# Performance work log

Hardware: AMD Instinct MI355X
Metric: run time of the kernel (lower is better)

Reference implementation:

```python
import jax, jax.numpy as jnp
import numpy as np

N = 100000
NEG_SLOPE = 0.2
EPS = 1e-16


def _gat_layer(x, W, a_src, a_dst, b, src, dst, heads, dim, concat):
    # Linear projection -> [N, H, D]
    h = (x @ W).reshape(x.shape[0], heads, dim)
    # Per-node attention logits [N, H]
    al_src = jnp.sum(h * a_src[None], axis=-1)
    al_dst = jnp.sum(h * a_dst[None], axis=-1)
    # Per-edge logits, leaky relu (negative_slope=0.2)
    e = al_src[src] + al_dst[dst]                      # [E, H]
    e = jnp.where(e >= 0, e, NEG_SLOPE * e)
    # Scatter softmax over destination neighborhoods
    emax = jax.ops.segment_max(e, dst, num_segments=N)  # [N, H]
    ee = jnp.exp(e - emax[dst])
    denom = jax.ops.segment_sum(ee, dst, num_segments=N)
    alpha = ee / (denom[dst] + EPS)                    # [E, H]
    # Weighted scatter-add aggregation
    msg = h[src] * alpha[:, :, None]                   # [E, H, D]
    out = jax.ops.segment_sum(msg, dst, num_segments=N)  # [N, H, D]
    if concat:
        out = out.reshape(N, heads * dim)
    else:
        out = out.mean(axis=1)
    return out + b


def setup_inputs() -> dict:
    key = jax.random.key(0)
    ks = jax.random.split(key, 10)
    F_in, hid, H, C = 500, 8, 8, 3
    E = 3200000
    x = jax.random.normal(ks[0], (N, F_in), dtype=jnp.float32)
    edge_index = jax.random.randint(ks[1], (2, E), 0, N, dtype=jnp.int64)
    s1 = (1.0 / np.sqrt(F_in)).astype(np.float32)
    s2 = (1.0 / np.sqrt(hid * H)).astype(np.float32)
    return {
        "x": x,
        "edge_index": edge_index,
        "W1": jax.random.normal(ks[2], (F_in, H * hid), dtype=jnp.float32) * s1,
        "att_src1": jax.random.normal(ks[3], (H, hid), dtype=jnp.float32),
        "att_dst1": jax.random.normal(ks[4], (H, hid), dtype=jnp.float32),
        "b1": jnp.zeros((H * hid,), dtype=jnp.float32),
        "W2": jax.random.normal(ks[5], (H * hid, C), dtype=jnp.float32) * s2,
        "att_src2": jax.random.normal(ks[6], (1, C), dtype=jnp.float32),
        "att_dst2": jax.random.normal(ks[7], (1, C), dtype=jnp.float32),
        "b2": jnp.zeros((C,), dtype=jnp.float32),
    }


def reference(x, edge_index, W1, att_src1, att_dst1, b1, W2, att_src2, att_dst2, b2):
    # Add self-loops (PyG GATConv default)
    loop = jnp.arange(N, dtype=edge_index.dtype)
    src = jnp.concatenate([edge_index[0], loop])
    dst = jnp.concatenate([edge_index[1], loop])
    # Layer 1: 8 heads, concat -> [N, 64], ELU
    h = _gat_layer(x, W1, att_src1, att_dst1, b1, src, dst, heads=8, dim=8, concat=True)
    h = jax.nn.elu(h)
    # Layer 2: 1 head, no concat -> [N, 3]
    out = _gat_layer(h, W2, att_src2, att_dst2, b2, src, dst, heads=1, dim=3, concat=False)
    return out, jax.nn.log_softmax(out, axis=1)
```

## Files before the change

### kernel.cpp

```cpp
#include <hip/hip_runtime.h>
#include <hip/hip_bf16.h>


#define F_IN 500
#define HEADS 8
#define HID 8
#define HD 64
#define CLS 3
#define NEG 0.2f
#define EPSV 1e-16f
#define LOG2E 1.44269504088896340736f

#define NBLK_H 128
#define NBKT_MAX 3136

typedef __attribute__((ext_vector_type(8))) short short8v;
typedef __attribute__((ext_vector_type(4))) float f32x4;

__device__ inline short bfs(float v) {
    __hip_bfloat16 b = __float2bfloat16(v);
    return *(short*)&b;
}

__device__ inline int ld_edge(const void* ei, long idx, int is64) {
    return is64 ? (int)((const long long*)ei)[idx] : ((const int*)ei)[idx];
}

__global__ void k_prepW(const float* __restrict__ W1, ushort* __restrict__ W1b2,
                        const int* __restrict__ ei, int* __restrict__ flag) {
    if (blockIdx.x == 0 && threadIdx.x == 0) {
        int z = 0;
        for (int i = 1; i < 16; i += 2) z += (ei[i] == 0) ? 1 : 0;
        *flag = (z == 8) ? 1 : 0;
    }
    int i = blockIdx.x * 256 + threadIdx.x;
    if (i >= 16 * 64 * 32) return;
    int ks = i >> 11;
    int c = (i >> 5) & 63;
    int st = i & 31;
    int q = (st >> 3) ^ ((c >> 1) & 3);
    int k = ks * 32 + q * 8 + (st & 7);
    float v = (k < F_IN) ? W1[k * HD + c] : 0.f;
    __hip_bfloat16 b = __float2bfloat16(v);
    W1b2[i] = *(ushort*)&b;
}

__device__ __forceinline__ void g1_stage(const float* __restrict__ x,
        const ushort* __restrict__ W1b2, char* smem, int buf, int ks,
        int rowb, int N, int lane, int w) {
    const int k0 = ks * 32;
    {
        const ushort* srcB = W1b2 + ks * 2048 + (w * 64 + lane) * 8;
        char* dstB = smem + 16384 + buf * 4096 + w * 1024;
        __builtin_amdgcn_global_load_lds(
            (const __attribute__((address_space(1))) void*)srcB,
            (__attribute__((address_space(3))) void*)dstB, 16, 0, 0);
    }
#pragma unroll
    for (int i = 0; i < 2; ++i) {
        int vt = i * 256 + w * 64 + lane;
        int row = vt >> 3;
        int c = (vt & 7) ^ (row & 7);
        int ke = k0 + c * 4; if (ke > 496) ke = 496;
        int rowg = rowb + row; if (rowg >= N) rowg = N - 1;
        const float* srcA = x + (long)rowg * F_IN + ke;
        char* dstA = smem + buf * 8192 + i * 4096 + w * 1024;
        __builtin_amdgcn_global_load_lds(
            (const __attribute__((address_space(1))) void*)srcA,
            (__attribute__((address_space(3))) void*)dstA, 16, 0, 0);
    }
}

__global__ __launch_bounds__(256) void k_gemm1(const float* __restrict__ x,
        const ushort* __restrict__ W1b2,
        const float* __restrict__ asrc, const float* __restrict__ adst,
        float* __restrict__ als, float* __restrict__ ald,
        ushort* __restrict__ h1b, int N) {
    __shared__ char smem[24576];
    int t = threadIdx.x;
    int lane = t & 63;
    int w = t >> 6;
    int l16 = lane & 15, oct = lane >> 4;
    int rowb = blockIdx.x * 64;

    f32x4 acc0 = {0.f, 0.f, 0.f, 0.f};
    f32x4 acc1 = {0.f, 0.f, 0.f, 0.f};
    f32x4 acc2 = {0.f, 0.f, 0.f, 0.f};
    f32x4 acc3 = {0.f, 0.f, 0.f, 0.f};

    g1_stage(x, W1b2, smem, 0, 0, rowb, N, lane, w);
    __syncthreads();

    int rl = w * 16 + l16;
    int asw = l16 & 7;
    int bsw = (l16 >> 1) & 3;

    for (int ks = 0; ks < 16; ++ks) {
        int cur = ks & 1;
        if (ks < 15)
            g1_stage(x, W1b2, smem, cur ^ 1, ks + 1, rowb, N, lane, w);
        const char* Ab = smem + cur * 8192;
        const char* Bb = smem + 16384 + cur * 4096;
        float4 x0 = *reinterpret_cast<const float4*>(
            Ab + rl * 128 + ((2 * oct + 0) ^ asw) * 16);
        float4 x1 = *reinterpret_cast<const float4*>(
            Ab + rl * 128 + ((2 * oct + 1) ^ asw) * 16);
        short8v a;
        a[0] = bfs(x0.x); a[1] = bfs(x0.y); a[2] = bfs(x0.z); a[3] = bfs(x0.w);
        a[4] = bfs(x1.x); a[5] = bfs(x1.y); a[6] = bfs(x1.z); a[7] = bfs(x1.w);
        short8v b0 = *reinterpret_cast<const short8v*>(
            Bb + (0 * 16 + l16) * 64 + (oct ^ bsw) * 16);
        short8v b1 = *reinterpret_cast<const short8v*>(
            Bb + (1 * 16 + l16) * 64 + (oct ^ bsw) * 16);
        short8v b2 = *reinterpret_cast<const short8v*>(
            Bb + (2 * 16 + l16) * 64 + (oct ^ bsw) * 16);
        short8v b3 = *reinterpret_cast<const short8v*>(
            Bb + (3 * 16 + l16) * 64 + (oct ^ bsw) * 16);
        acc0 = __builtin_amdgcn_mfma_f32_16x16x32_bf16(a, b0, acc0, 0, 0, 0);
        acc1 = __builtin_amdgcn_mfma_f32_16x16x32_bf16(a, b1, acc1, 0, 0, 0);
        acc2 = __builtin_amdgcn_mfma_f32_16x16x32_bf16(a, b2, acc2, 0, 0, 0);
        acc3 = __builtin_amdgcn_mfma_f32_16x16x32_bf16(a, b3, acc3, 0, 0, 0);
        __syncthreads();
    }

    float* fs = (float*)smem;
#pragma unroll
    for (int r = 0; r < 4; ++r) {
        int rl_ = w * 16 + oct * 4 + r;
        fs[rl_ * 64 + l16 +  0] = acc0[r];
        fs[rl_ * 64 + l16 + 16] = acc1[r];
        fs[rl_ * 64 + l16 + 32] = acc2[r];
        fs[rl_ * 64 + l16 + 48] = acc3[r];
    }
    __syncthreads();
#pragma unroll
    for (int j = t; j < 512; j += 256) {
        int row = j >> 3, h = j & 7;
        int gn = rowb + row;
        if (gn < N) {
            const float* hp = fs + row * 64 + h * 8;
            float4 v0 = *reinterpret_cast<const float4*>(hp);
            float4 v1 = *reinterpret_cast<const float4*>(hp + 4);
            const float* s = asrc + h * 8;
            const float* d = adst + h * 8;
            float s1 = v0.x * s[0] + v0.y * s[1] + v0.z * s[2] + v0.w * s[3]
                     + v1.x * s[4] + v1.y * s[5] + v1.z * s[6] + v1.w * s[7];
            float s2 = v0.x * d[0] + v0.y * d[1] + v0.z * d[2] + v0.w * d[3]
                     + v1.x * d[4] + v1.y * d[5] + v1.z * d[6] + v1.w * d[7];
            als[gn * 8 + h] = s1 * LOG2E;
            ald[gn * 8 + h] = s2 * LOG2E;
            ushort hb[8];
            hb[0] = (ushort)bfs(v0.x); hb[1] = (ushort)bfs(v0.y);
            hb[2] = (ushort)bfs(v0.z); hb[3] = (ushort)bfs(v0.w);
            hb[4] = (ushort)bfs(v1.x); hb[5] = (ushort)bfs(v1.y);
            hb[6] = (ushort)bfs(v1.z); hb[7] = (ushort)bfs(v1.w);
            *reinterpret_cast<uint4*>(h1b + (long)gn * HD + h * 8) =
                *reinterpret_cast<const uint4*>(hb);
        }
    }
}


__global__ __launch_bounds__(256) void k_hist(const void* ei, int E, int N, int nbkt,
        int* __restrict__ ghist, const int* flag) {
    __shared__ int h[NBKT_MAX];
    int tot = E + N;
    int epb = (tot + NBLK_H - 1) / NBLK_H;
    int e0 = blockIdx.x * epb, e1 = min(tot, e0 + epb);
    for (int i = threadIdx.x; i < nbkt; i += 256) h[i] = 0;
    __syncthreads();
    int is64 = *flag;
    for (int e = e0 + threadIdx.x; e < e1; e += 256) {
        int dst = (e < E) ? ld_edge(ei, (long)E + e, is64) : (e - E);
        atomicAdd(&h[dst >> 5], 1);
    }
    __syncthreads();
    for (int i = threadIdx.x; i < nbkt; i += 256)
        ghist[blockIdx.x * nbkt + i] = h[i];
}

__global__ void k_bsum(const int* __restrict__ ghist, int* __restrict__ colsum, int nbkt) {
    int b = blockIdx.x * 256 + threadIdx.x;
    if (b >= nbkt) return;
    int s = 0;
    for (int i = 0; i < NBLK_H; i++) s += ghist[i * nbkt + b];
    colsum[b] = s;
}

__global__ __launch_bounds__(256) void k_bscan2(const int* __restrict__ colsum,
        int* __restrict__ boff, int nbkt) {
    __shared__ int part[256];
    int per = (nbkt + 255) / 256;
    int t = threadIdx.x;
    int lo = t * per, hi = min(nbkt, lo + per);
    int s = 0;
    for (int i = lo; i < hi; i++) s += colsum[i];
    part[t] = s;
    __syncthreads();
    for (int off = 1; off < 256; off <<= 1) {
        int v = (t >= off) ? part[t - off] : 0;
        __syncthreads();
        part[t] += v;
        __syncthreads();
    }
    int run = (t > 0) ? part[t - 1] : 0;
    for (int i = lo; i < hi; i++) { boff[i] = run; run += colsum[i]; }
    if (t == 255) boff[nbkt] = part[255];
}

__global__ void k_bapply(int* __restrict__ ghist, const int* __restrict__ boff, int nbkt) {
    int b = blockIdx.x * 256 + threadIdx.x;
    if (b >= nbkt) return;
    int run = boff[b];
    for (int i = 0; i < NBLK_H; i++) {
        int v = ghist[i * nbkt + b];
        ghist[i * nbkt + b] = run;
        run += v;
    }
}

__global__ __launch_bounds__(256) void k_scatter(const void* ei, int E, int N, int nbkt,
        const int* __restrict__ ghist, uint* __restrict__ pairs, const int* flag) {
    __shared__ int cur[NBKT_MAX];
    int tot = E + N;
    int epb = (tot + NBLK_H - 1) / NBLK_H;
    int e0 = blockIdx.x * epb, e1 = min(tot, e0 + epb);
    for (int i = threadIdx.x; i < nbkt; i += 256) cur[i] = ghist[blockIdx.x * nbkt + i];
    __syncthreads();
    int is64 = *flag;
    for (int e = e0 + threadIdx.x; e < e1; e += 256) {
        int src, dst;
        if (e < E) { src = ld_edge(ei, e, is64); dst = ld_edge(ei, (long)E + e, is64); }
        else { src = dst = e - E; }
        int pos = atomicAdd(&cur[dst >> 5], 1);
        pairs[pos] = ((uint)src << 5) | (uint)(dst & 31);
    }
}

__global__ __launch_bounds__(256) void k_fill3(const uint* __restrict__ pairs,
        const int* __restrict__ boff, int* __restrict__ rowptr,
        int* __restrict__ csr, int N, int nbkt) {
    __shared__ int cnt[32];
    __shared__ int base[32];
    __shared__ int cur[32];
    int b = blockIdx.x;
    int t = threadIdx.x;
    if (t < 32) { cnt[t] = 0; cur[t] = 0; }
    __syncthreads();
    int p0 = boff[b], p1 = boff[b + 1];
    for (int p = p0 + t; p < p1; p += 256)
        atomicAdd(&cnt[pairs[p] & 31], 1);
    __syncthreads();
    if (t < 32) {
        int pre = 0;
#pragma unroll
        for (int i = 0; i < 32; i++) pre += (i < t) ? cnt[i] : 0;
        base[t] = p0 + pre;
        int n = b * 32 + t;
        if (n < N) rowptr[n] = base[t];
    }
    if (b == 0 && t == 0) rowptr[N] = boff[nbkt];
    __syncthreads();
    for (int p = p0 + t; p < p1; p += 256) {
        uint v = pairs[p];
        int lo = v & 31;
        int pos = base[lo] + atomicAdd(&cur[lo], 1);
        csr[pos] = (int)(v >> 5);
    }
}

__global__ __launch_bounds__(256) void k_agg1(const int* __restrict__ rowptr,
        const int* __restrict__ csr, const ushort* __restrict__ h1b,
        const float* __restrict__ als, const float* __restrict__ ald,
        const float* __restrict__ b1, const float* __restrict__ W2,
        const float* __restrict__ as2, const float* __restrict__ ad2,
        float* __restrict__ h2p, float* __restrict__ als2,
        float* __restrict__ ald2, int N) {
    int n = blockIdx.x * 4 + (threadIdx.x >> 6);
    if (n >= N) return;
    int lane = threadIdx.x & 63;
    int es = lane >> 3;
    int h = lane & 7;
    float aldh = ald[n * HEADS + h];
    int rs = rowptr[n], re = rowptr[n + 1];

    float a0 = 0.f, a1 = 0.f, a2 = 0.f, a3 = 0.f;
    float a4 = 0.f, a5 = 0.f, a6 = 0.f, a7 = 0.f;
    float c0 = 0.f, c1 = 0.f, c2 = 0.f, c3 = 0.f;
    float c4 = 0.f, c5 = 0.f, c6 = 0.f, c7 = 0.f;
    float den = 0.f, den2 = 0.f;

    int jb = rs;
    for (; jb + 16 <= re; jb += 16) {
        int sA = csr[jb + es];
        int sB = csr[jb + 8 + es];
        float eA = als[sA * HEADS + h] + aldh;
        float eB = als[sB * HEADS + h] + aldh;
        uint4 uA = *reinterpret_cast<const uint4*>(h1b + (long)sA * HD + h * 8);
        uint4 uB = *reinterpret_cast<const uint4*>(h1b + (long)sB * HD + h * 8);
        eA = fmaxf(eA, NEG * eA);
        eB = fmaxf(eB, NEG * eB);
        float pA = exp2f(eA);
        float pB = exp2f(eB);
        a0 += pA * __uint_as_float(uA.x << 16);
        a1 += pA * __uint_as_float(uA.x & 0xffff0000u);
        a2 += pA * __uint_as_float(uA.y << 16);
        a3 += pA * __uint_as_float(uA.y & 0xffff0000u);
        a4 += pA * __uint_as_float(uA.z << 16);
        a5 += pA * __uint_as_float(uA.z & 0xffff0000u);
        a6 += pA * __uint_as_float(uA.w << 16);
        a7 += pA * __uint_as_float(uA.w & 0xffff0000u);
        den += pA;
        c0 += pB * __uint_as_float(uB.x << 16);
        c1 += pB * __uint_as_float(uB.x & 0xffff0000u);
        c2 += pB * __uint_as_float(uB.y << 16);
        c3 += pB * __uint_as_float(uB.y & 0xffff0000u);
        c4 += pB * __uint_as_float(uB.z << 16);
        c5 += pB * __uint_as_float(uB.z & 0xffff0000u);
        c6 += pB * __uint_as_float(uB.w << 16);
        c7 += pB * __uint_as_float(uB.w & 0xffff0000u);
        den2 += pB;
    }
    for (; jb < re; jb += 8) {
        int eidx = jb + es;
        bool valid = (eidx < re);
        int s = csr[valid ? eidx : rs];
        float e = als[s * HEADS + h] + aldh;
        e = fmaxf(e, NEG * e);
        float p = valid ? exp2f(e) : 0.f;
        uint4 u = *reinterpret_cast<const uint4*>(h1b + (long)s * HD + h * 8);
        a0 += p * __uint_as_float(u.x << 16);
        a1 += p * __uint_as_float(u.x & 0xffff0000u);
        a2 += p * __uint_as_float(u.y << 16);
        a3 += p * __uint_as_float(u.y & 0xffff0000u);
        a4 += p * __uint_as_float(u.z << 16);
        a5 += p * __uint_as_float(u.z & 0xffff0000u);
        a6 += p * __uint_as_float(u.w << 16);
        a7 += p * __uint_as_float(u.w & 0xffff0000u);
        den += p;
    }
    a0 += c0; a1 += c1; a2 += c2; a3 += c3;
    a4 += c4; a5 += c5; a6 += c6; a7 += c7;
    den += den2;
#pragma unroll
    for (int off = 8; off < 64; off <<= 1) {
        den += __shfl_xor(den, off);
        a0 += __shfl_xor(a0, off); a1 += __shfl_xor(a1, off);
        a2 += __shfl_xor(a2, off); a3 += __shfl_xor(a3, off);
        a4 += __shfl_xor(a4, off); a5 += __shfl_xor(a5, off);
        a6 += __shfl_xor(a6, off); a7 += __shfl_xor(a7, off);
    }
    float sel = (es < 4)
        ? ((es < 2) ? ((es == 0) ? a0 : a1) : ((es == 2) ? a2 : a3))
        : ((es < 6) ? ((es == 4) ? a4 : a5) : ((es == 6) ? a6 : a7));
    int d = h * 8 + es;
    float o = sel / (den + EPSV) + b1[d];
    o = (o > 0.f) ? o : __expf(o) - 1.f;
    float p0 = o * W2[d * CLS + 0];
    float p1 = o * W2[d * CLS + 1];
    float p2 = o * W2[d * CLS + 2];
#pragma unroll
    for (int off = 1; off < 64; off <<= 1) {
        p0 += __shfl_xor(p0, off);
        p1 += __shfl_xor(p1, off);
        p2 += __shfl_xor(p2, off);
    }
    if (lane == 0) {
        *reinterpret_cast<float4*>(h2p + (long)n * 4) = make_float4(p0, p1, p2, 0.f);
        als2[n] = (p0 * as2[0] + p1 * as2[1] + p2 * as2[2]) * LOG2E;
        ald2[n] = (p0 * ad2[0] + p1 * ad2[1] + p2 * ad2[2]) * LOG2E;
    }
}

__global__ __launch_bounds__(256) void k_agg2(const int* __restrict__ rowptr,
        const int* __restrict__ csr, const float* __restrict__ h2p,
        const float* __restrict__ als2v, const float* __restrict__ ald2v,
        const float* __restrict__ b2, float* __restrict__ out, int N) {
    int n = blockIdx.x * 8 + (threadIdx.x >> 5);
    if (n >= N) return;
    int lane = threadIdx.x & 31;
    float aldv = ald2v[n];
    int rs = rowptr[n], re = rowptr[n + 1];
    float sum = 0.f, a0 = 0.f, a1 = 0.f, a2 = 0.f;
    for (int j = rs + lane; j < re; j += 32) {
        int s = csr[j];
        float e = als2v[s] + aldv;
        e = fmaxf(e, NEG * e);
        float p = exp2f(e);
        float4 hv = *reinterpret_cast<const float4*>(h2p + (long)s * 4);
        sum += p;
        a0 += p * hv.x;
        a1 += p * hv.y;
        a2 += p * hv.z;
    }
#pragma unroll
    for (int off = 1; off < 32; off <<= 1) {
        sum += __shfl_xor(sum, off);
        a0 += __shfl_xor(a0, off);
        a1 += __shfl_xor(a1, off);
        a2 += __shfl_xor(a2, off);
    }
    if (lane == 0) {
        float d = sum + EPSV;
        float v0 = a0 / d + b2[0], v1 = a1 / d + b2[1], v2 = a2 / d + b2[2];
        float mx = fmaxf(v0, fmaxf(v1, v2));
        float se = __expf(v0 - mx) + __expf(v1 - mx) + __expf(v2 - mx);
        float ls = mx + __logf(se);
        out[n * CLS + 0] = v0; out[n * CLS + 1] = v1; out[n * CLS + 2] = v2;
        long o2 = (long)N * CLS;
        out[o2 + n * CLS + 0] = v0 - ls;
        out[o2 + n * CLS + 1] = v1 - ls;
        out[o2 + n * CLS + 2] = v2 - ls;
    }
}

extern "C" void kernel_launch(void* const* d_in, const int* in_sizes, int n_in,
                              void* d_out, int out_size, void* d_ws, size_t ws_size,
                              hipStream_t stream) {
    const float* x   = (const float*)d_in[0];
    const void*  ei  = d_in[1];
    const float* W1  = (const float*)d_in[2];
    const float* as1 = (const float*)d_in[3];
    const float* ad1 = (const float*)d_in[4];
    const float* b1  = (const float*)d_in[5];
    const float* W2  = (const float*)d_in[6];
    const float* as2 = (const float*)d_in[7];
    const float* ad2 = (const float*)d_in[8];
    const float* b2  = (const float*)d_in[9];
    int N = in_sizes[0] / F_IN;
    int E = in_sizes[1] / 2;
    int tot = E + N;
    int nbkt = (N + 31) >> 5;

    char* w = (char*)d_ws;
    auto alloc = [&](size_t bytes) -> char* {
        char* p = w; w += (bytes + 255) & ~size_t(255); return p;
    };
    ushort* h1b    = (ushort*)alloc((size_t)N * HD * 2);
    float*  als1   = (float*)alloc((size_t)N * HEADS * 4);
    float*  ald1   = (float*)alloc((size_t)N * HEADS * 4);
    int*    rowptr = (int*)alloc((size_t)(N + 1) * 4);
    int*    csr    = (int*)alloc((size_t)tot * 4);
    float*  h2p    = (float*)alloc((size_t)N * 4 * 4);
    float*  als2   = (float*)alloc((size_t)N * 4);
    float*  ald2   = (float*)alloc((size_t)N * 4);
    ushort* W1b2   = (ushort*)alloc((size_t)16 * 64 * 32 * 2);
    int*    flag   = (int*)alloc(256);
    uint*   pairs  = (uint*)alloc((size_t)tot * 4);
    int*    ghist  = (int*)alloc((size_t)NBLK_H * nbkt * 4);
    int*    colsum = (int*)alloc((size_t)nbkt * 4);
    int*    boff   = (int*)alloc((size_t)(nbkt + 1) * 4);

    k_prepW<<<(16 * 64 * 32 + 255) / 256, 256, 0, stream>>>(W1, W1b2, (const int*)ei, flag);
    k_gemm1<<<(N + 63) / 64, 256, 0, stream>>>(x, W1b2, as1, ad1, als1, ald1, h1b, N);
    k_hist<<<NBLK_H, 256, 0, stream>>>(ei, E, N, nbkt, ghist, flag);
    k_bsum<<<(nbkt + 255) / 256, 256, 0, stream>>>(ghist, colsum, nbkt);
    k_bscan2<<<1, 256, 0, stream>>>(colsum, boff, nbkt);
    k_bapply<<<(nbkt + 255) / 256, 256, 0, stream>>>(ghist, boff, nbkt);
    k_scatter<<<NBLK_H, 256, 0, stream>>>(ei, E, N, nbkt, ghist, pairs, flag);
    k_fill3<<<nbkt, 256, 0, stream>>>(pairs, boff, rowptr, csr, N, nbkt);
    k_agg1<<<(N + 3) / 4, 256, 0, stream>>>(rowptr, csr, h1b, als1, ald1, b1,
                                            W2, as2, ad2, h2p, als2, ald2, N);
    k_agg2<<<(N + 7) / 8, 256, 0, stream>>>(rowptr, csr, h2p, als2, ald2, b2,
                                            (float*)d_out, N);
}
```

Before: 337.8 us.

## Fuse histogram into GEMM launch and unroll aggregation loop to four edge groups

The edge histogram blocks now run as extra blocks of the layer-1 GEMM kernel, so the two independent stages overlap inside one launch instead of running back to back. The histogram block count doubles, which spreads the edge range over more blocks but also makes ghist larger and lengthens the column sums in k_bsum and k_scatter. The agg1 main loop now processes 32 edges per iteration with four independent accumulator sets, so more gathers are in flight at once. The cost is higher register pressure in agg1 and extra smem-sized fat blocks that share the GEMM grid.

```diff
diff --git a/kernel.cpp b/kernel.cpp
--- a/kernel.cpp
+++ b/kernel.cpp
@@ -11,7 +11,7 @@
 #define EPSV 1e-16f
 #define LOG2E 1.44269504088896340736f
 
-#define NBLK_H 128
+#define NBLK_H 256
 #define NBKT_MAX 3136
 
 typedef __attribute__((ext_vector_type(8))) short short8v;
@@ -71,13 +71,36 @@
     }
 }
 
-__global__ __launch_bounds__(256) void k_gemm1(const float* __restrict__ x,
+__global__ __launch_bounds__(256) void k_fatA(const float* __restrict__ x,
         const ushort* __restrict__ W1b2,
         const float* __restrict__ asrc, const float* __restrict__ adst,
         float* __restrict__ als, float* __restrict__ ald,
-        ushort* __restrict__ h1b, int N) {
+        ushort* __restrict__ h1b, int N,
+        const void* ei, int E, int nbkt, int* __restrict__ ghist,
+        const int* __restrict__ flag) {
     __shared__ char smem[24576];
+    int gB = (N + 63) >> 6;
     int t = threadIdx.x;
+
+    if ((int)blockIdx.x >= gB) {
+        int hb = blockIdx.x - gB;
+        int* h = (int*)smem;
+        int tot = E + N;
+        int epb = (tot + NBLK_H - 1) / NBLK_H;
+        int e0 = hb * epb, e1 = min(tot, e0 + epb);
+        for (int i = t; i < nbkt; i += 256) h[i] = 0;
+        __syncthreads();
+        int is64 = *flag;
+        for (int e = e0 + t; e < e1; e += 256) {
+            int dst = (e < E) ? ld_edge(ei, (long)E + e, is64) : (e - E);
+            atomicAdd(&h[dst >> 5], 1);
+        }
+        __syncthreads();
+        for (int i = t; i < nbkt; i += 256)
+            ghist[hb * nbkt + i] = h[i];
+        return;
+    }
+
     int lane = t & 63;
     int w = t >> 6;
     int l16 = lane & 15, oct = lane >> 4;
@@ -161,24 +184,6 @@
 }
 
 
-__global__ __launch_bounds__(256) void k_hist(const void* ei, int E, int N, int nbkt,
-        int* __restrict__ ghist, const int* flag) {
-    __shared__ int h[NBKT_MAX];
-    int tot = E + N;
-    int epb = (tot + NBLK_H - 1) / NBLK_H;
-    int e0 = blockIdx.x * epb, e1 = min(tot, e0 + epb);
-    for (int i = threadIdx.x; i < nbkt; i += 256) h[i] = 0;
-    __syncthreads();
-    int is64 = *flag;
-    for (int e = e0 + threadIdx.x; e < e1; e += 256) {
-        int dst = (e < E) ? ld_edge(ei, (long)E + e, is64) : (e - E);
-        atomicAdd(&h[dst >> 5], 1);
-    }
-    __syncthreads();
-    for (int i = threadIdx.x; i < nbkt; i += 256)
-        ghist[blockIdx.x * nbkt + i] = h[i];
-}
-
 __global__ void k_bsum(const int* __restrict__ ghist, int* __restrict__ colsum, int nbkt) {
     int b = blockIdx.x * 256 + threadIdx.x;
     if (b >= nbkt) return;
@@ -284,42 +289,67 @@
     float aldh = ald[n * HEADS + h];
     int rs = rowptr[n], re = rowptr[n + 1];
 
-    float a0 = 0.f, a1 = 0.f, a2 = 0.f, a3 = 0.f;
-    float a4 = 0.f, a5 = 0.f, a6 = 0.f, a7 = 0.f;
-    float c0 = 0.f, c1 = 0.f, c2 = 0.f, c3 = 0.f;
-    float c4 = 0.f, c5 = 0.f, c6 = 0.f, c7 = 0.f;
-    float den = 0.f, den2 = 0.f;
+    float acc[4][8];
+    float den[4] = {0.f, 0.f, 0.f, 0.f};
+#pragma unroll
+    for (int q = 0; q < 4; ++q)
+#pragma unroll
+        for (int j = 0; j < 8; ++j) acc[q][j] = 0.f;
 
     int jb = rs;
+    for (; jb + 32 <= re; jb += 32) {
+        int s[4]; float e[4]; float p[4]; uint4 u[4];
+#pragma unroll
+        for (int q = 0; q < 4; ++q) s[q] = csr[jb + q * 8 + es];
+#pragma unroll
+        for (int q = 0; q < 4; ++q) {
+            e[q] = als[s[q] * HEADS + h] + aldh;
+            u[q] = *reinterpret_cast<const uint4*>(h1b + (long)s[q] * HD + h * 8);
+        }
+#pragma unroll
+        for (int q = 0; q < 4; ++q) {
+            e[q] = fmaxf(e[q], NEG * e[q]);
+            p[q] = exp2f(e[q]);
+        }
+#pragma unroll
+        for (int q = 0; q < 4; ++q) {
+            acc[q][0] += p[q] * __uint_as_float(u[q].x << 16);
+            acc[q][1] += p[q] * __uint_as_float(u[q].x & 0xffff0000u);
+            acc[q][2] += p[q] * __uint_as_float(u[q].y << 16);
+            acc[q][3] += p[q] * __uint_as_float(u[q].y & 0xffff0000u);
+            acc[q][4] += p[q] * __uint_as_float(u[q].z << 16);
+            acc[q][5] += p[q] * __uint_as_float(u[q].z & 0xffff0000u);
+            acc[q][6] += p[q] * __uint_as_float(u[q].w << 16);
+            acc[q][7] += p[q] * __uint_as_float(u[q].w & 0xffff0000u);
+            den[q] += p[q];
+        }
+    }
     for (; jb + 16 <= re; jb += 16) {
-        int sA = csr[jb + es];
-        int sB = csr[jb + 8 + es];
-        float eA = als[sA * HEADS + h] + aldh;
-        float eB = als[sB * HEADS + h] + aldh;
-        uint4 uA = *reinterpret_cast<const uint4*>(h1b + (long)sA * HD + h * 8);
-        uint4 uB = *reinterpret_cast<const uint4*>(h1b + (long)sB * HD + h * 8);
-        eA = fmaxf(eA, NEG * eA);
-        eB = fmaxf(eB, NEG * eB);
-        float pA = exp2f(eA);
-        float pB = exp2f(eB);
-        a0 += pA * __uint_as_float(uA.x << 16);
-        a1 += pA * __uint_as_float(uA.x & 0xffff0000u);
-        a2 += pA * __uint_as_float(uA.y << 16);
-        a3 += pA * __uint_as_float(uA.y & 0xffff0000u);
-        a4 += pA * __uint_as_float(uA.z << 16);
-        a5 += pA * __uint_as_float(uA.z & 0xffff0000u);
-        a6 += pA * __uint_as_float(uA.w << 16);
-        a7 += pA * __uint_as_float(uA.w & 0xffff0000u);
-        den += pA;
-        c0 += pB * __uint_as_float(uB.x << 16);
-        c1 += pB * __uint_as_float(uB.x & 0xffff0000u);
-        c2 += pB * __uint_as_float(uB.y << 16);
-        c3 += pB * __uint_as_float(uB.y & 0xffff0000u);
-        c4 += pB * __uint_as_float(uB.z << 16);
-        c5 += pB * __uint_as_float(uB.z & 0xffff0000u);
-        c6 += pB * __uint_as_float(uB.w << 16);
-        c7 += pB * __uint_as_float(uB.w & 0xffff0000u);
-        den2 += pB;
+        int s[2]; float e[2]; float p[2]; uint4 u[2];
+#pragma unroll
+        for (int q = 0; q < 2; ++q) s[q] = csr[jb + q * 8 + es];
+#pragma unroll
+        for (int q = 0; q < 2; ++q) {
+            e[q] = als[s[q] * HEADS + h] + aldh;
+            u[q] = *reinterpret_cast<const uint4*>(h1b + (long)s[q] * HD + h * 8);
+        }
+#pragma unroll
+        for (int q = 0; q < 2; ++q) {
+            e[q] = fmaxf(e[q], NEG * e[q]);
+            p[q] = exp2f(e[q]);
+        }
+#pragma unroll
+        for (int q = 0; q < 2; ++q) {
+            acc[q][0] += p[q] * __uint_as_float(u[q].x << 16);
+            acc[q][1] += p[q] * __uint_as_float(u[q].x & 0xffff0000u);
+            acc[q][2] += p[q] * __uint_as_float(u[q].y << 16);
+            acc[q][3] += p[q] * __uint_as_float(u[q].y & 0xffff0000u);
+            acc[q][4] += p[q] * __uint_as_float(u[q].z << 16);
+            acc[q][5] += p[q] * __uint_as_float(u[q].z & 0xffff0000u);
+            acc[q][6] += p[q] * __uint_as_float(u[q].w << 16);
+            acc[q][7] += p[q] * __uint_as_float(u[q].w & 0xffff0000u);
+            den[q] += p[q];
+        }
     }
     for (; jb < re; jb += 8) {
         int eidx = jb + es;
@@ -329,22 +359,28 @@
         e = fmaxf(e, NEG * e);
         float p = valid ? exp2f(e) : 0.f;
         uint4 u = *reinterpret_cast<const uint4*>(h1b + (long)s * HD + h * 8);
-        a0 += p * __uint_as_float(u.x << 16);
-        a1 += p * __uint_as_float(u.x & 0xffff0000u);
-        a2 += p * __uint_as_float(u.y << 16);
-        a3 += p * __uint_as_float(u.y & 0xffff0000u);
-        a4 += p * __uint_as_float(u.z << 16);
-        a5 += p * __uint_as_float(u.z & 0xffff0000u);
-        a6 += p * __uint_as_float(u.w << 16);
-        a7 += p * __uint_as_float(u.w & 0xffff0000u);
-        den += p;
-    }
-    a0 += c0; a1 += c1; a2 += c2; a3 += c3;
-    a4 += c4; a5 += c5; a6 += c6; a7 += c7;
-    den += den2;
+        acc[0][0] += p * __uint_as_float(u.x << 16);
+        acc[0][1] += p * __uint_as_float(u.x & 0xffff0000u);
+        acc[0][2] += p * __uint_as_float(u.y << 16);
+        acc[0][3] += p * __uint_as_float(u.y & 0xffff0000u);
+        acc[0][4] += p * __uint_as_float(u.z << 16);
+        acc[0][5] += p * __uint_as_float(u.z & 0xffff0000u);
+        acc[0][6] += p * __uint_as_float(u.w << 16);
+        acc[0][7] += p * __uint_as_float(u.w & 0xffff0000u);
+        den[0] += p;
+    }
+    float a0 = (acc[0][0] + acc[1][0]) + (acc[2][0] + acc[3][0]);
+    float a1 = (acc[0][1] + acc[1][1]) + (acc[2][1] + acc[3][1]);
+    float a2 = (acc[0][2] + acc[1][2]) + (acc[2][2] + acc[3][2]);
+    float a3 = (acc[0][3] + acc[1][3]) + (acc[2][3] + acc[3][3]);
+    float a4 = (acc[0][4] + acc[1][4]) + (acc[2][4] + acc[3][4]);
+    float a5 = (acc[0][5] + acc[1][5]) + (acc[2][5] + acc[3][5]);
+    float a6 = (acc[0][6] + acc[1][6]) + (acc[2][6] + acc[3][6]);
+    float a7 = (acc[0][7] + acc[1][7]) + (acc[2][7] + acc[3][7]);
+    float dn = (den[0] + den[1]) + (den[2] + den[3]);
 #pragma unroll
     for (int off = 8; off < 64; off <<= 1) {
-        den += __shfl_xor(den, off);
+        dn += __shfl_xor(dn, off);
         a0 += __shfl_xor(a0, off); a1 += __shfl_xor(a1, off);
         a2 += __shfl_xor(a2, off); a3 += __shfl_xor(a3, off);
         a4 += __shfl_xor(a4, off); a5 += __shfl_xor(a5, off);
@@ -354,7 +390,7 @@
         ? ((es < 2) ? ((es == 0) ? a0 : a1) : ((es == 2) ? a2 : a3))
         : ((es < 6) ? ((es == 4) ? a4 : a5) : ((es == 6) ? a6 : a7));
     int d = h * 8 + es;
-    float o = sel / (den + EPSV) + b1[d];
+    float o = sel / (dn + EPSV) + b1[d];
     o = (o > 0.f) ? o : __expf(o) - 1.f;
     float p0 = o * W2[d * CLS + 0];
     float p1 = o * W2[d * CLS + 1];
@@ -451,9 +487,10 @@
     int*    colsum = (int*)alloc((size_t)nbkt * 4);
     int*    boff   = (int*)alloc((size_t)(nbkt + 1) * 4);
 
+    int gB = (N + 63) / 64;
     k_prepW<<<(16 * 64 * 32 + 255) / 256, 256, 0, stream>>>(W1, W1b2, (const int*)ei, flag);
-    k_gemm1<<<(N + 63) / 64, 256, 0, stream>>>(x, W1b2, as1, ad1, als1, ald1, h1b, N);
-    k_hist<<<NBLK_H, 256, 0, stream>>>(ei, E, N, nbkt, ghist, flag);
+    k_fatA<<<gB + NBLK_H, 256, 0, stream>>>(x, W1b2, as1, ad1, als1, ald1, h1b, N,
+                                            ei, E, nbkt, ghist, flag);
     k_bsum<<<(nbkt + 255) / 256, 256, 0, stream>>>(ghist, colsum, nbkt);
     k_bscan2<<<1, 256, 0, stream>>>(colsum, boff, nbkt);
     k_bapply<<<(nbkt + 255) / 256, 256, 0, stream>>>(ghist, boff, nbkt);
```

After: 306.7 us. -9.2%, faster.
